# Kernel tuning notes

Measured on AMD Instinct MI355X. Metric: run time of the kernel, lower is better.

The kernel has to match this reference:

```python
import jax, jax.numpy as jnp
import numpy as np

NUM_EMBEDDINGS = 1024
EMBEDDING_DIM = 256
COMMITMENT_COST = 0.25


def setup_inputs() -> dict:
    key = jax.random.key(0)
    k1, k2 = jax.random.split(key)
    z = jax.random.normal(k1, (65536, EMBEDDING_DIM), dtype=jnp.float32)
    # embeddings.weight.data.uniform_(-1/K, 1/K)
    codebook = jax.random.uniform(
        k2, (NUM_EMBEDDINGS, EMBEDDING_DIM), dtype=jnp.float32,
        minval=-1.0 / NUM_EMBEDDINGS, maxval=1.0 / NUM_EMBEDDINGS)
    return {"z": z, "codebook": codebook}


def reference(z, codebook):
    B, D = z.shape
    K = codebook.shape[0]
    # ||z - e||^2 = ||z||^2 - 2 z.e + ||e||^2  (avoids (B,K,D) intermediate)
    z_sq = jnp.sum(z * z, axis=1, keepdims=True)            # (B,1)
    e_sq = jnp.sum(codebook * codebook, axis=1)             # (K,)
    distances = z_sq - 2.0 * (z @ codebook.T) + e_sq[None, :]  # (B,K)
    encoding_indices = jnp.argmin(distances, axis=1)        # (B,)
    # one-hot @ weight == direct gather
    z_q = codebook[encoding_indices]                        # (B,D)

    loss_codebook = jnp.mean((jax.lax.stop_gradient(z_q) - z) ** 2)
    loss_commit = jnp.mean((z_q - jax.lax.stop_gradient(z)) ** 2)

    counts = jnp.zeros((K,), dtype=jnp.float32).at[encoding_indices].add(1.0)
    avg_probs = counts / B
    perplexity = jnp.exp(-jnp.sum(avg_probs * jnp.log(avg_probs + 1e-10)))

    target_perplexity = K * 0.1
    perplexity_ratio = jnp.clip(target_perplexity / (perplexity + 1e-10), 0.0, 10.0)
    diversity_loss = perplexity_ratio * 0.1
    vq_loss = loss_codebook + COMMITMENT_COST * loss_commit + diversity_loss

    # straight-through estimator
    z_q_st = z + jax.lax.stop_gradient(z_q - z)
    return z_q_st, vq_loss, perplexity
```

## Files before the change

### kernel.cpp

```cpp
#include <hip/hip_runtime.h>
#include <math.h>

#define NROWS 65536
#define NCODES 1024
#define DIM 256
#define BM 64
#define CCH 256
#define NCC 4
#define BK 64
#define NKC 4
#define FLAG_CAP 8192
#define FLAG_GAP 3e-4f

typedef _Float16 h8 __attribute__((ext_vector_type(8)));
typedef _Float16 h4 __attribute__((ext_vector_type(4)));
typedef float f32x4 __attribute__((ext_vector_type(4)));

struct Flag { int row; int i1; int i2; };

__device__ __forceinline__ void gl_lds16(void* lds, const void* g) {
    __builtin_amdgcn_global_load_lds(
        (const __attribute__((address_space(1))) unsigned int*)g,
        (__attribute__((address_space(3))) unsigned int*)lds, 16, 0, 0);
}

__global__ __launch_bounds__(256)
void prep_z_kernel(const float* __restrict__ z, char* __restrict__ outb,
                   float* __restrict__ z_sq) {
    const int l = threadIdx.x & 63;
    const int w = threadIdx.x >> 6;
    const int wave = blockIdx.x * 4 + w;
#pragma unroll 4
    for (int i = 0; i < 16; ++i) {
        int row = wave * 16 + i;
        float4 v = ((const float4*)(z + (size_t)row * DIM))[l];
        float ss = v.x * v.x + v.y * v.y + v.z * v.z + v.w * v.w;
        h4 hv = { (_Float16)v.x, (_Float16)v.y, (_Float16)v.z, (_Float16)v.w };
        *(h4*)(outb + (size_t)row * 1024 + l * 8) = hv;
#pragma unroll
        for (int off = 32; off > 0; off >>= 1) ss += __shfl_down(ss, off);
        if (l == 0) z_sq[row] = ss;
    }
}

__global__ __launch_bounds__(256)
void prep_cb_kernel(const float* __restrict__ cb, char* __restrict__ f_hi,
                    float* __restrict__ esq) {
    const int l = threadIdx.x & 63;
    const int w = threadIdx.x >> 6;
    const int code = blockIdx.x * 4 + w;
    float4 v = ((const float4*)(cb + (size_t)code * DIM))[l];
    float ss = v.x * v.x + v.y * v.y + v.z * v.z + v.w * v.w;
    h4 hv = { (_Float16)(v.x * 1024.f), (_Float16)(v.y * 1024.f),
              (_Float16)(v.z * 1024.f), (_Float16)(v.w * 1024.f) };
    *(h4*)(f_hi + (size_t)code * 512 + l * 8) = hv;
#pragma unroll
    for (int off = 32; off > 0; off >>= 1) ss += __shfl_down(ss, off);
    if (l == 0) esq[code] = ss;
}

__global__ __launch_bounds__(256, 4)
void gemm_argmin_kernel(const char* __restrict__ zhib,
                        const char* __restrict__ f_hi,
                        const float* __restrict__ esq,
                        const float* __restrict__ z_sq,
                        const float* __restrict__ cb,
                        float* __restrict__ out,
                        int* __restrict__ hist, float* __restrict__ loss_sum,
                        int* __restrict__ cnt, Flag* __restrict__ flags) {
    __shared__ __align__(16) char arena[40960];
    const int tid = threadIdx.x;
    const int w = tid >> 6;
    const int l = tid & 63;
    const int l15 = l & 15;
    const int lhi = l >> 4;
    const int b0 = blockIdx.x * BM;

    const h8* zLh = (const h8*)(arena);
    const h8* cLh = (const h8*)(arena + 8192);

    float top_b[4], top_s[4];
#pragma unroll
    for (int i = 0; i < 4; ++i) { top_b[i] = INFINITY; top_s[i] = INFINITY; }

    for (int cc = 0; cc < NCC; ++cc) {
        f32x4 acc[4][4];
#pragma unroll
        for (int i = 0; i < 4; ++i)
#pragma unroll
            for (int j = 0; j < 4; ++j) acc[i][j] = (f32x4){0.f, 0.f, 0.f, 0.f};

        for (int kc = 0; kc < NKC; ++kc) {
            __syncthreads();
#pragma unroll
            for (int q = 0; q < 2; ++q) {
                int ch = w * 2 + q;
                int row = ch * 8 + (l >> 3);
                const char* src = zhib + (size_t)(b0 + row) * 1024 + kc * 128 + (l & 7) * 16;
                gl_lds16(arena + ch * 1024, src);
            }
#pragma unroll
            for (int q = 0; q < 8; ++q) {
                int ch = w * 8 + q;
                int crow = ch * 8 + (l >> 3);
                const char* src = f_hi + (size_t)(cc * CCH + crow) * 512 + kc * 128 + (l & 7) * 16;
                gl_lds16(arena + 8192 + ch * 1024, src);
            }
            __syncthreads();

#pragma unroll
            for (int s = 0; s < 2; ++s) {
                h8 bfr[4];
#pragma unroll
                for (int fz = 0; fz < 4; ++fz)
                    bfr[fz] = zLh[(fz * 16 + l15) * 8 + s * 4 + lhi];
#pragma unroll
                for (int fc = 0; fc < 4; ++fc) {
                    h8 afr = cLh[(w * 64 + fc * 16 + l15) * 8 + s * 4 + lhi];
#pragma unroll
                    for (int fz = 0; fz < 4; ++fz)
                        acc[fc][fz] = __builtin_amdgcn_mfma_f32_16x16x32_f16(
                            afr, bfr[fz], acc[fc][fz], 0, 0, 0);
                }
            }
        }
#pragma unroll
        for (int fc = 0; fc < 4; ++fc) {
#pragma unroll
            for (int r = 0; r < 4; ++r) {
                int code = cc * CCH + w * 64 + fc * 16 + lhi * 4 + r;
                float es = esq[code];
#pragma unroll
                for (int fz = 0; fz < 4; ++fz) {
                    float dist = fmaf(acc[fc][fz][r], -0.001953125f, es);
                    float p = __uint_as_float((__float_as_uint(dist) & ~1023u) | (unsigned)code);
                    top_s[fz] = fminf(top_s[fz], fmaxf(top_b[fz], p));
                    top_b[fz] = fminf(top_b[fz], p);
                }
            }
        }
    }

    __syncthreads();
#pragma unroll
    for (int fz = 0; fz < 4; ++fz) {
        int row = fz * 16 + l15;
        int entry = w * 4 + lhi;
        *(float2*)(arena + row * 128 + entry * 8) = make_float2(top_b[fz], top_s[fz]);
    }
    __syncthreads();
    int* bidx = (int*)(arena + 8192);
    if (tid < BM) {
        float b = INFINITY, s2 = INFINITY;
#pragma unroll
        for (int e = 0; e < 16; ++e) {
            float2 v = *(float2*)(arena + tid * 128 + e * 8);
            s2 = fminf(fminf(s2, v.y), fmaxf(b, v.x));
            b = fminf(b, v.x);
        }
        unsigned ib = __float_as_uint(b) & 1023u;
        bidx[tid] = (int)ib;
        atomicAdd(&hist[ib], 1);
        float lr = z_sq[b0 + tid] + b;
#pragma unroll
        for (int off = 32; off > 0; off >>= 1) lr += __shfl_down(lr, off);
        if (tid == 0) atomicAdd(loss_sum, lr);
        if (s2 - b < FLAG_GAP) {
            int pos = atomicAdd(cnt, 1);
            if (pos < FLAG_CAP) {
                flags[pos].row = b0 + tid;
                flags[pos].i1 = (int)ib;
                flags[pos].i2 = (int)(__float_as_uint(s2) & 1023u);
            }
        }
    }
    __syncthreads();
    {
        int row = tid >> 2, q = tid & 3;
        int ib = bidx[row];
        const float4* src = (const float4*)(cb + (size_t)ib * DIM + q * 64);
        float4* dst = (float4*)(out + (size_t)(b0 + row) * DIM + q * 64);
#pragma unroll
        for (int i = 0; i < 16; ++i) dst[i] = src[i];
    }
}

__global__ __launch_bounds__(256)
void rescue_kernel(const float* __restrict__ z, const float* __restrict__ cb,
                   const int* __restrict__ cnt, const Flag* __restrict__ flags,
                   float* __restrict__ out, int* __restrict__ hist,
                   float* __restrict__ loss_sum) {
    int n = *cnt; if (n > FLAG_CAP) n = FLAG_CAP;
    const int l = threadIdx.x & 63;
    const int wave = (blockIdx.x * blockDim.x + threadIdx.x) >> 6;
    const int nw = (gridDim.x * blockDim.x) >> 6;
    for (int f = wave; f < n; f += nw) {
        Flag fl = flags[f];
        float4 zv = ((const float4*)(z + (size_t)fl.row * DIM))[l];
        float4 a = ((const float4*)(cb + (size_t)fl.i1 * DIM))[l];
        float4 b = ((const float4*)(cb + (size_t)fl.i2 * DIM))[l];
        double s1 = (double)a.x * (a.x - 2.0 * zv.x) + (double)a.y * (a.y - 2.0 * zv.y)
                  + (double)a.z * (a.z - 2.0 * zv.z) + (double)a.w * (a.w - 2.0 * zv.w);
        double s2 = (double)b.x * (b.x - 2.0 * zv.x) + (double)b.y * (b.y - 2.0 * zv.y)
                  + (double)b.z * (b.z - 2.0 * zv.z) + (double)b.w * (b.w - 2.0 * zv.w);
#pragma unroll
        for (int off = 32; off > 0; off >>= 1) {
            s1 += __shfl_down(s1, off);
            s2 += __shfl_down(s2, off);
        }
        s1 = __shfl(s1, 0);
        s2 = __shfl(s2, 0);
        int win2 = (s2 < s1) || (s2 == s1 && fl.i2 < fl.i1);
        if (win2) {
            ((float4*)(out + (size_t)fl.row * DIM))[l] = b;
            if (l == 0) {
                atomicAdd(&hist[fl.i2], 1);
                atomicAdd(&hist[fl.i1], -1);
                atomicAdd(loss_sum, (float)(s2 - s1));
            }
        }
    }
}

__global__ __launch_bounds__(256)
void vq_final_kernel(const int* __restrict__ hist, const float* __restrict__ loss_sum,
                     float* __restrict__ out) {
    int tid = threadIdx.x;
    float s = 0.f;
    for (int t = tid; t < NCODES; t += 256) {
        float p = (float)hist[t] * (1.0f / 65536.f);
        s += p * logf(p + 1e-10f);
    }
#pragma unroll
    for (int off = 32; off > 0; off >>= 1) s += __shfl_down(s, off);
    __shared__ float wsum[4];
    if ((tid & 63) == 0) wsum[tid >> 6] = s;
    __syncthreads();
    if (tid == 0) {
        float tot = wsum[0] + wsum[1] + wsum[2] + wsum[3];
        float perp = expf(-tot);
        float mse = loss_sum[0] * (1.0f / 16777216.f);
        float ratio = 102.4f / (perp + 1e-10f);
        ratio = fminf(fmaxf(ratio, 0.f), 10.f);
        out[(size_t)NROWS * DIM] = 1.25f * mse + 0.1f * ratio;
        out[(size_t)NROWS * DIM + 1] = perp;
    }
}

extern "C" void kernel_launch(void* const* d_in, const int* in_sizes, int n_in,
                              void* d_out, int out_size, void* d_ws, size_t ws_size,
                              hipStream_t stream) {
    const float* z = (const float*)d_in[0];
    const float* cb = (const float*)d_in[1];
    float* out = (float*)d_out;
    char* ws = (char*)d_ws;

    int*   hist  = (int*)(ws + 0);
    float* loss  = (float*)(ws + 4096);
    int*   cnt   = (int*)(ws + 4100);
    float* esq   = (float*)(ws + 8192);
    float* z_sq  = (float*)(ws + 12288);
    Flag*  flags = (Flag*)(ws + 274432);
    char*  f_hi  = ws + 372736;

    hipMemsetAsync(ws, 0, 4104, stream);
    prep_z_kernel<<<1024, 256, 0, stream>>>(z, (char*)d_out, z_sq);
    prep_cb_kernel<<<256, 256, 0, stream>>>(cb, f_hi, esq);
    gemm_argmin_kernel<<<NROWS / BM, 256, 0, stream>>>(
        (const char*)d_out, f_hi, esq, z_sq, cb, out, hist, loss, cnt, flags);
    rescue_kernel<<<32, 256, 0, stream>>>(z, cb, cnt, flags, out, hist, loss);
    vq_final_kernel<<<1, 256, 0, stream>>>(hist, loss, out);
}
```

Measured before the change: 266.2 us.

## Keep z fragments in registers and double-buffer swizzled codebook tiles

The GEMM-argmin kernel now loads a 128-row z block once into registers and streams 64-code codebook tiles through a double-buffered LDS ring with async global-to-LDS loads and vmcnt waits, instead of reloading both operands per K chunk. The prep kernels write fp16 data with an XOR swizzle so that LDS fragment reads avoid bank conflicts. The cross-wave top-2 reduction through LDS is replaced by intra-wave shuffles, since each wave now covers all codes for its own rows, and esq is staged in LDS. The trade-off is heavier register and LDS use, with occupancy lowered from 4 to 2 blocks per CU.

```diff
diff --git a/kernel.cpp b/kernel.cpp
--- a/kernel.cpp
+++ b/kernel.cpp
@@ -4,11 +4,9 @@
 #define NROWS 65536
 #define NCODES 1024
 #define DIM 256
-#define BM 64
-#define CCH 256
-#define NCC 4
-#define BK 64
-#define NKC 4
+#define BM 128
+#define TCODES 64
+#define NTILES 16
 #define FLAG_CAP 8192
 #define FLAG_GAP 3e-4f
 
@@ -36,7 +34,8 @@
         float4 v = ((const float4*)(z + (size_t)row * DIM))[l];
         float ss = v.x * v.x + v.y * v.y + v.z * v.z + v.w * v.w;
         h4 hv = { (_Float16)v.x, (_Float16)v.y, (_Float16)v.z, (_Float16)v.w };
-        *(h4*)(outb + (size_t)row * 1024 + l * 8) = hv;
+        int col = (l * 8) ^ ((row & 7) << 4);
+        *(h4*)(outb + (size_t)row * 1024 + col) = hv;
 #pragma unroll
         for (int off = 32; off > 0; off >>= 1) ss += __shfl_down(ss, off);
         if (l == 0) z_sq[row] = ss;
@@ -53,22 +52,30 @@
     float ss = v.x * v.x + v.y * v.y + v.z * v.z + v.w * v.w;
     h4 hv = { (_Float16)(v.x * 1024.f), (_Float16)(v.y * 1024.f),
               (_Float16)(v.z * 1024.f), (_Float16)(v.w * 1024.f) };
-    *(h4*)(f_hi + (size_t)code * 512 + l * 8) = hv;
+    int col = (l * 8) ^ ((code & 7) << 4);
+    *(h4*)(f_hi + (size_t)code * 512 + col) = hv;
 #pragma unroll
     for (int off = 32; off > 0; off >>= 1) ss += __shfl_down(ss, off);
     if (l == 0) esq[code] = ss;
 }
 
-__global__ __launch_bounds__(256, 4)
+#define STAGE(bo, tile) do {                                                   \
+    _Pragma("unroll")                                                          \
+    for (int i_ = 0; i_ < 8; ++i_)                                             \
+        gl_lds16(arena + (bo) + i_ * 4096 + tid * 16,                          \
+                 f_hi + (size_t)(tile) * 32768 + i_ * 4096 + tid * 16);        \
+} while (0)
+
+__global__ __launch_bounds__(256, 2)
 void gemm_argmin_kernel(const char* __restrict__ zhib,
                         const char* __restrict__ f_hi,
-                        const float* __restrict__ esq,
+                        const float* __restrict__ esq_g,
                         const float* __restrict__ z_sq,
                         const float* __restrict__ cb,
                         float* __restrict__ out,
                         int* __restrict__ hist, float* __restrict__ loss_sum,
                         int* __restrict__ cnt, Flag* __restrict__ flags) {
-    __shared__ __align__(16) char arena[40960];
+    __shared__ __align__(16) char arena[70144];
     const int tid = threadIdx.x;
     const int w = tid >> 6;
     const int l = tid & 63;
@@ -76,112 +83,119 @@
     const int lhi = l >> 4;
     const int b0 = blockIdx.x * BM;
 
-    const h8* zLh = (const h8*)(arena);
-    const h8* cLh = (const h8*)(arena + 8192);
-
-    float top_b[4], top_s[4];
-#pragma unroll
-    for (int i = 0; i < 4; ++i) { top_b[i] = INFINITY; top_s[i] = INFINITY; }
-
-    for (int cc = 0; cc < NCC; ++cc) {
-        f32x4 acc[4][4];
-#pragma unroll
-        for (int i = 0; i < 4; ++i)
-#pragma unroll
-            for (int j = 0; j < 4; ++j) acc[i][j] = (f32x4){0.f, 0.f, 0.f, 0.f};
-
-        for (int kc = 0; kc < NKC; ++kc) {
-            __syncthreads();
-#pragma unroll
-            for (int q = 0; q < 2; ++q) {
-                int ch = w * 2 + q;
-                int row = ch * 8 + (l >> 3);
-                const char* src = zhib + (size_t)(b0 + row) * 1024 + kc * 128 + (l & 7) * 16;
-                gl_lds16(arena + ch * 1024, src);
-            }
-#pragma unroll
-            for (int q = 0; q < 8; ++q) {
-                int ch = w * 8 + q;
-                int crow = ch * 8 + (l >> 3);
-                const char* src = f_hi + (size_t)(cc * CCH + crow) * 512 + kc * 128 + (l & 7) * 16;
-                gl_lds16(arena + 8192 + ch * 1024, src);
-            }
-            __syncthreads();
-
-#pragma unroll
-            for (int s = 0; s < 2; ++s) {
-                h8 bfr[4];
-#pragma unroll
-                for (int fz = 0; fz < 4; ++fz)
-                    bfr[fz] = zLh[(fz * 16 + l15) * 8 + s * 4 + lhi];
-#pragma unroll
-                for (int fc = 0; fc < 4; ++fc) {
-                    h8 afr = cLh[(w * 64 + fc * 16 + l15) * 8 + s * 4 + lhi];
-#pragma unroll
-                    for (int fz = 0; fz < 4; ++fz)
-                        acc[fc][fz] = __builtin_amdgcn_mfma_f32_16x16x32_f16(
-                            afr, bfr[fz], acc[fc][fz], 0, 0, 0);
+    gl_lds16(arena + 65536 + tid * 16, esq_g + tid * 4);
+#pragma unroll
+    for (int i = 0; i < 16; ++i) {
+        int L = i * 4096 + tid * 16;
+        gl_lds16(arena + L, zhib + (size_t)(b0 + (L >> 9)) * 1024 + (L & 511));
+    }
+    __syncthreads();
+
+    h8 zf0[8], zf1[8];
+#pragma unroll
+    for (int s = 0; s < 8; ++s) {
+        const int r0 = w * 32 + l15;
+        const int r1 = w * 32 + 16 + l15;
+        zf0[s] = *(const h8*)(arena + r0 * 512 + ((64 * s + 16 * lhi) ^ ((r0 & 7) << 4)));
+        zf1[s] = *(const h8*)(arena + r1 * 512 + ((64 * s + 16 * lhi) ^ ((r1 & 7) << 4)));
+    }
+    __syncthreads();
+
+    const float* esqL = (const float*)(arena + 65536);
+    float topb0 = INFINITY, tops0 = INFINITY, topb1 = INFINITY, tops1 = INFINITY;
+
+    STAGE(0, 0);
+    STAGE(32768, 1);
+
+    for (int t = 0; t < NTILES; ++t) {
+        const int bo = (t & 1) << 15;
+        if (t == NTILES - 1) { asm volatile("s_waitcnt vmcnt(0)" ::: "memory"); }
+        else                 { asm volatile("s_waitcnt vmcnt(8)" ::: "memory"); }
+        __builtin_amdgcn_s_barrier();
+
+        f32x4 acc[4][2];
+#pragma unroll
+        for (int fc = 0; fc < 4; ++fc) {
+            acc[fc][0] = (f32x4){0.f, 0.f, 0.f, 0.f};
+            acc[fc][1] = (f32x4){0.f, 0.f, 0.f, 0.f};
+        }
+#pragma unroll
+        for (int s = 0; s < 8; ++s) {
+#pragma unroll
+            for (int fc = 0; fc < 4; ++fc) {
+                const int cl = fc * 16 + l15;
+                h8 afr = *(const h8*)(arena + bo + cl * 512 +
+                                      ((64 * s + 16 * lhi) ^ ((cl & 7) << 4)));
+                acc[fc][0] = __builtin_amdgcn_mfma_f32_16x16x32_f16(afr, zf0[s], acc[fc][0], 0, 0, 0);
+                acc[fc][1] = __builtin_amdgcn_mfma_f32_16x16x32_f16(afr, zf1[s], acc[fc][1], 0, 0, 0);
+            }
+        }
+        __builtin_amdgcn_sched_barrier(0);
+        __builtin_amdgcn_s_barrier();
+        if (t < NTILES - 2) STAGE(bo, t + 2);
+
+#pragma unroll
+        for (int fc = 0; fc < 4; ++fc) {
+#pragma unroll
+            for (int r = 0; r < 4; ++r) {
+                const int code = t * 64 + fc * 16 + lhi * 4 + r;
+                const float es = esqL[code];
+                float d0 = fmaf(acc[fc][0][r], -0.001953125f, es);
+                float d1 = fmaf(acc[fc][1][r], -0.001953125f, es);
+                float p0 = __uint_as_float((__float_as_uint(d0) & ~1023u) | (unsigned)code);
+                float p1 = __uint_as_float((__float_as_uint(d1) & ~1023u) | (unsigned)code);
+                tops0 = fminf(tops0, fmaxf(topb0, p0));
+                topb0 = fminf(topb0, p0);
+                tops1 = fminf(tops1, fmaxf(topb1, p1));
+                topb1 = fminf(topb1, p1);
+            }
+        }
+    }
+
+#pragma unroll
+    for (int m = 16; m <= 32; m <<= 1) {
+        float ob = __shfl_xor(topb0, m, 64), os = __shfl_xor(tops0, m, 64);
+        tops0 = fminf(fminf(tops0, os), fmaxf(topb0, ob));
+        topb0 = fminf(topb0, ob);
+        ob = __shfl_xor(topb1, m, 64); os = __shfl_xor(tops1, m, 64);
+        tops1 = fminf(fminf(tops1, os), fmaxf(topb1, ob));
+        topb1 = fminf(topb1, ob);
+    }
+
+    int* bidx = (int*)(arena + 69632);
+    float lr = 0.f;
+    if (lhi == 0) {
+#pragma unroll
+        for (int fz = 0; fz < 2; ++fz) {
+            const float b = fz ? topb1 : topb0;
+            const float s2 = fz ? tops1 : tops0;
+            const int row = w * 32 + fz * 16 + l15;
+            const unsigned ib = __float_as_uint(b) & 1023u;
+            bidx[row] = (int)ib;
+            atomicAdd(&hist[ib], 1);
+            lr += z_sq[b0 + row] + __uint_as_float(__float_as_uint(b) & ~1023u);
+            if (s2 - b < FLAG_GAP) {
+                int pos = atomicAdd(cnt, 1);
+                if (pos < FLAG_CAP) {
+                    flags[pos].row = b0 + row;
+                    flags[pos].i1 = (int)ib;
+                    flags[pos].i2 = (int)(__float_as_uint(s2) & 1023u);
                 }
             }
         }
-#pragma unroll
-        for (int fc = 0; fc < 4; ++fc) {
-#pragma unroll
-            for (int r = 0; r < 4; ++r) {
-                int code = cc * CCH + w * 64 + fc * 16 + lhi * 4 + r;
-                float es = esq[code];
-#pragma unroll
-                for (int fz = 0; fz < 4; ++fz) {
-                    float dist = fmaf(acc[fc][fz][r], -0.001953125f, es);
-                    float p = __uint_as_float((__float_as_uint(dist) & ~1023u) | (unsigned)code);
-                    top_s[fz] = fminf(top_s[fz], fmaxf(top_b[fz], p));
-                    top_b[fz] = fminf(top_b[fz], p);
-                }
-            }
-        }
-    }
-
-    __syncthreads();
-#pragma unroll
-    for (int fz = 0; fz < 4; ++fz) {
-        int row = fz * 16 + l15;
-        int entry = w * 4 + lhi;
-        *(float2*)(arena + row * 128 + entry * 8) = make_float2(top_b[fz], top_s[fz]);
-    }
-    __syncthreads();
-    int* bidx = (int*)(arena + 8192);
-    if (tid < BM) {
-        float b = INFINITY, s2 = INFINITY;
-#pragma unroll
-        for (int e = 0; e < 16; ++e) {
-            float2 v = *(float2*)(arena + tid * 128 + e * 8);
-            s2 = fminf(fminf(s2, v.y), fmaxf(b, v.x));
-            b = fminf(b, v.x);
-        }
-        unsigned ib = __float_as_uint(b) & 1023u;
-        bidx[tid] = (int)ib;
-        atomicAdd(&hist[ib], 1);
-        float lr = z_sq[b0 + tid] + b;
-#pragma unroll
-        for (int off = 32; off > 0; off >>= 1) lr += __shfl_down(lr, off);
-        if (tid == 0) atomicAdd(loss_sum, lr);
-        if (s2 - b < FLAG_GAP) {
-            int pos = atomicAdd(cnt, 1);
-            if (pos < FLAG_CAP) {
-                flags[pos].row = b0 + tid;
-                flags[pos].i1 = (int)ib;
-                flags[pos].i2 = (int)(__float_as_uint(s2) & 1023u);
-            }
-        }
-    }
+    }
+#pragma unroll
+    for (int off = 32; off > 0; off >>= 1) lr += __shfl_down(lr, off, 64);
+    if (l == 0) atomicAdd(loss_sum, lr);
+
     __syncthreads();
     {
-        int row = tid >> 2, q = tid & 3;
-        int ib = bidx[row];
-        const float4* src = (const float4*)(cb + (size_t)ib * DIM + q * 64);
-        float4* dst = (float4*)(out + (size_t)(b0 + row) * DIM + q * 64);
-#pragma unroll
-        for (int i = 0; i < 16; ++i) dst[i] = src[i];
+        const int row = tid >> 1, q = tid & 1;
+        const int ib = bidx[row];
+        const float4* src = (const float4*)(cb + (size_t)ib * DIM + q * 128);
+        float4* dst = (float4*)(out + (size_t)(b0 + row) * DIM + q * 128);
+#pragma unroll
+        for (int i = 0; i < 32; ++i) dst[i] = src[i];
     }
 }
 
```

After: 260.4 us. 2.2% less time.
